# Kernel optimization log

Measured on AMD Instinct MI355X. Metric: run time of the kernel, lower is better.

## Reference

```python
import jax, jax.numpy as jnp
import numpy as np

B, G, T, N = 2, 4, 64, 300
D = 256          # detr_dim == feature_dim
R = 4            # ffn_dim_ratio
MD = 32          # motion_dim


def _xavier(key, shape):
    lim = (6.0 / (shape[0] + shape[1])) ** 0.5
    return jax.random.uniform(key, shape, jnp.float32, -lim, lim)


def setup_inputs() -> dict:
    key = jax.random.key(0)
    ks = jax.random.split(key, 16)
    feats = jax.random.normal(ks[0], (B, G, T, N, D), jnp.float32)
    boxes = jax.random.uniform(ks[1], (B, G, T, N, 4), jnp.float32)
    masks = jax.random.bernoulli(ks[2], 0.3, (B, G, T, N))
    # per-trajectory permutation of frame ids 0..T-1 (unique -> unambiguous scatter)
    u = jax.random.uniform(ks[3], (B, G, N, T))
    times = jnp.swapaxes(jnp.argsort(u, axis=-1).astype(jnp.int32), 2, 3)  # [B,G,T,N]
    return {
        'trajectory_features': feats,
        'trajectory_boxes': boxes,
        'trajectory_masks': masks,
        'trajectory_times': times,
        'adp_w1': _xavier(ks[4], (D, D * R)), 'adp_b1': jnp.zeros((D * R,), jnp.float32),
        'adp_w2': _xavier(ks[5], (D * R, D)), 'adp_b2': jnp.zeros((D,), jnp.float32),
        'norm_g': jnp.ones((D,), jnp.float32), 'norm_b': jnp.zeros((D,), jnp.float32),
        'mot_w1': _xavier(ks[6], (12, MD // 2)), 'mot_b1': jnp.zeros((MD // 2,), jnp.float32),
        'mot_w2': _xavier(ks[7], (MD // 2, MD)), 'mot_b2': jnp.zeros((MD,), jnp.float32),
        'fus_w1': _xavier(ks[8], (D + MD, D)), 'fus_b1': jnp.zeros((D,), jnp.float32),
        'fus_w2': _xavier(ks[9], (D, D)), 'fus_b2': jnp.zeros((D,), jnp.float32),
        'ffn_w1': _xavier(ks[10], (D, D * R)), 'ffn_b1': jnp.zeros((D * R,), jnp.float32),
        'ffn_w2': _xavier(ks[11], (D * R, D)), 'ffn_b2': jnp.zeros((D,), jnp.float32),
        'fnorm_g': jnp.ones((D,), jnp.float32), 'fnorm_b': jnp.zeros((D,), jnp.float32),
    }


def _ffn(x, w1, b1, w2, b2):
    return jax.nn.gelu(x @ w1 + b1, approximate=False) @ w2 + b2


def _ln(x, g, b):
    m = x.mean(-1, keepdims=True)
    v = ((x - m) ** 2).mean(-1, keepdims=True)
    return (x - m) / jnp.sqrt(v + 1e-5) * g + b


def _motion_features(boxes, masks, times, mot_w1, mot_b1, mot_w2, mot_b2):
    # boxes [B,G,T,N,4] -> trajectory-major [B,G,N,T,*]
    b_, g_, t_, n_ = masks.shape
    md = mot_b2.shape[0]
    bx = jnp.swapaxes(boxes, 2, 3)              # [B,G,N,T,4]
    valid = ~jnp.swapaxes(masks, 2, 3)          # [B,G,N,T]
    tm = jnp.swapaxes(times, 2, 3)              # [B,G,N,T]
    # sort valid entries first, by time (stable)
    order = jnp.argsort(jnp.where(valid, tm, t_ + 1), axis=-1)
    sb = jnp.take_along_axis(bx, order[..., None], axis=3)   # sorted boxes
    st = jnp.take_along_axis(tm, order, axis=-1)             # sorted times
    cnt = valid.sum(-1)                                      # [B,G,N]
    pos = jnp.arange(t_)
    in_count = pos[None, None, None, :] < cnt[..., None]
    dt = jnp.maximum(st - jnp.roll(st, 1, axis=-1), 1).astype(sb.dtype)[..., None]
    mask_v = ((pos >= 1)[None, None, None, :] & in_count)[..., None]
    vel = jnp.where(mask_v, (sb - jnp.roll(sb, 1, axis=3)) / dt, 0.0)
    mask_a = ((pos >= 2)[None, None, None, :] & in_count)[..., None]
    acc = jnp.where(mask_a, (vel - jnp.roll(vel, 1, axis=3)) / dt, 0.0)
    mv = jnp.concatenate([sb, vel, acc], axis=-1)            # [B,G,N,T,12]
    enc = jax.nn.gelu(mv @ mot_w1 + mot_b1, approximate=False) @ mot_w2 + mot_b2
    write = in_count & (cnt >= 2)[..., None] & (st < t_)
    frame = jnp.where(write, st, t_)                         # t_ -> dropped
    bi, gi, ni, ti = jnp.meshgrid(jnp.arange(b_), jnp.arange(g_), jnp.arange(n_),
                                  jnp.arange(t_), indexing='ij')
    out = jnp.zeros((b_, g_, t_, n_, md), sb.dtype)
    return out.at[bi, gi, frame, ni].set(enc, mode='drop')


def reference(trajectory_features, trajectory_boxes, trajectory_masks, trajectory_times,
              adp_w1, adp_b1, adp_w2, adp_b2, norm_g, norm_b,
              mot_w1, mot_b1, mot_w2, mot_b2,
              fus_w1, fus_b1, fus_w2, fus_b2,
              ffn_w1, ffn_b1, ffn_w2, ffn_b2, fnorm_g, fnorm_b):
    x = trajectory_features + _ffn(trajectory_features, adp_w1, adp_b1, adp_w2, adp_b2)
    x = _ln(x, norm_g, norm_b)
    motion = _motion_features(trajectory_boxes, trajectory_masks, trajectory_times,
                              mot_w1, mot_b1, mot_w2, mot_b2)
    cat = jnp.concatenate([x, motion], axis=-1)
    fused = jax.nn.gelu(cat @ fus_w1 + fus_b1, approximate=False) @ fus_w2 + fus_b2
    fused = fused + _ffn(fused, ffn_w1, ffn_b1, ffn_w2, ffn_b2)
    fused = _ln(fused, fnorm_g, fnorm_b)
    return fused, motion
```

## Files before the change

kernel.cpp:

```cpp
#include <hip/hip_runtime.h>

typedef __bf16 bf16x8 __attribute__((ext_vector_type(8)));
typedef float f32x4 __attribute__((ext_vector_type(4)));

namespace {

constexpr int T_ = 64;
constexpr int N_ = 300;
constexpr int MD_ = 32;
constexpr int BG_ = 8;
constexpr long MROWS_ = (long)BG_ * T_ * N_;
constexpr long FUSED_N = MROWS_ * 256;
constexpr int MB = 128;

constexpr long PA1 = 0;
constexpr long PA2 = 262144;
constexpr long PF1 = 524288;
constexpr long PF2 = 598016;
constexpr long PN1 = 663552;
constexpr long PN2 = 925696;

__device__ __forceinline__ float gelu_f(float x) {
  const float x2 = x * x;
  const float z2 = x * fmaf(x2, 0.07135481627f, 1.5957691216f);
  const float t = __builtin_amdgcn_rcpf(1.0f + __expf(z2));
  return x * (1.0f - t);
}

__device__ __forceinline__ float gelu_exact(float x) {
  return 0.5f * x * (1.0f + erff(x * 0.7071067811865476f));
}

__global__ void k_zero_flag(int* f) { *f = 0; }

__global__ void k_detect_mask(const unsigned char* __restrict__ m, int nbytes,
                              int* __restrict__ f) {
  int i = blockIdx.x * 256 + threadIdx.x;
  if (i < nbytes && (i & 3) != 0 && m[i] != 0) atomicOr(f, 1);
}

__global__ __launch_bounds__(256)
void k_motion(const float* __restrict__ boxes, const void* __restrict__ masks,
              const int* __restrict__ times,
              const float* __restrict__ mw1, const float* __restrict__ mb1,
              const float* __restrict__ mw2, const float* __restrict__ mb2,
              float* __restrict__ motion, const int* __restrict__ flagp) {
  __shared__ int slot[4][T_];
  __shared__ int sts[4][T_];
  __shared__ float sbx[4][T_][4];
  __shared__ float otile[4][T_][MD_];
  const int tid = threadIdx.x;
  const int w = tid >> 6, l = tid & 63;
  const int traj = blockIdx.x * 4 + w;
  const int bg = traj / N_, n = traj - bg * N_;
  const int isbool = *flagp;
  const long idx = ((long)bg * T_ + l) * N_ + n;
  const bool msk = isbool ? (((const unsigned char*)masks)[idx] != 0)
                          : (((const int*)masks)[idx] != 0);
  const bool valid = !msk;
  const int tm = times[idx];

  slot[w][l] = -1;
  sts[w][l] = 0;
  *(float4*)&sbx[w][l][0] = make_float4(0.f, 0.f, 0.f, 0.f);
  __syncthreads();
  if (valid) slot[w][tm] = l;
  __syncthreads();

  const int ot = slot[w][l];
  const bool vp = ot >= 0;
  const unsigned long long bal = __ballot(vp);
  const int cnt = __builtin_popcountll(bal);
  const int pos = __builtin_popcountll(bal & ((1ull << l) - 1ull));
  if (vp) {
    sts[w][pos] = l;
    const float4 bx = *(const float4*)(boxes + (((long)bg * T_ + ot) * N_ + n) * 4);
    *(float4*)&sbx[w][pos][0] = bx;
  }
  __syncthreads();

  const int stp = sts[w][l];
  const int stm1 = sts[w][(l + 63) & 63];
  const float4 sb = *(const float4*)&sbx[w][l][0];
  const float4 sbm = *(const float4*)&sbx[w][(l + 63) & 63][0];
  const float dt = (float)max(stp - stm1, 1);
  const float inv = 1.0f / dt;
  const bool okv = (l >= 1) && (l < cnt);
  float v0 = okv ? (sb.x - sbm.x) * inv : 0.f;
  float v1 = okv ? (sb.y - sbm.y) * inv : 0.f;
  float v2 = okv ? (sb.z - sbm.z) * inv : 0.f;
  float v3 = okv ? (sb.w - sbm.w) * inv : 0.f;
  const float p0 = __shfl_up(v0, 1, 64);
  const float p1 = __shfl_up(v1, 1, 64);
  const float p2 = __shfl_up(v2, 1, 64);
  const float p3 = __shfl_up(v3, 1, 64);
  const bool oka = (l >= 2) && (l < cnt);
  const float a0 = oka ? (v0 - p0) * inv : 0.f;
  const float a1 = oka ? (v1 - p1) * inv : 0.f;
  const float a2 = oka ? (v2 - p2) * inv : 0.f;
  const float a3 = oka ? (v3 - p3) * inv : 0.f;

  const float mv[12] = {sb.x, sb.y, sb.z, sb.w, v0, v1, v2, v3, a0, a1, a2, a3};
  float e1[16];
#pragma unroll
  for (int i = 0; i < 16; ++i) {
    float a = mb1[i];
#pragma unroll
    for (int c = 0; c < 12; ++c) a = fmaf(mv[c], mw1[c * 16 + i], a);
    e1[i] = gelu_exact(a);
  }
  float enc[32];
#pragma unroll
  for (int o = 0; o < 32; ++o) {
    float a = mb2[o];
#pragma unroll
    for (int i = 0; i < 16; ++i) a = fmaf(e1[i], mw2[i * 32 + o], a);
    enc[o] = a;
  }

#pragma unroll
  for (int c = 0; c < 32; c += 4)
    *(float4*)&otile[w][l][c] = make_float4(0.f, 0.f, 0.f, 0.f);
  __syncthreads();
  if (l < cnt && cnt >= 2) {
#pragma unroll
    for (int c = 0; c < 32; ++c) otile[w][stp][c] = enc[c];
  }
  __syncthreads();

  float* mbase = motion + ((long)bg * T_ * N_ + n) * MD_;
  const float4* srcv = (const float4*)&otile[w][l][0];
  float4* dstv = (float4*)(mbase + (long)l * N_ * MD_);
#pragma unroll
  for (int q = 0; q < 8; ++q) dstv[q] = srcv[q];
}

__global__ void k_pack(const float* __restrict__ W, __bf16* __restrict__ P,
                       int K, int NN) {
  int gid = blockIdx.x * 256 + threadIdx.x;
  int total = (K >> 5) * (NN >> 4) * 64;
  if (gid >= total) return;
  int l = gid & 63, f = gid >> 6;
  int NT = NN >> 4;
  int kb = f / NT, nt = f - kb * NT;
  int krow = kb * 32 + (l >> 4) * 8;
  int col = nt * 16 + (l & 15);
  bf16x8 v;
#pragma unroll
  for (int e = 0; e < 8; ++e) v[e] = (__bf16)W[(long)(krow + e) * NN + col];
  *(bf16x8*)(P + (long)gid * 8) = v;
}

__global__ __launch_bounds__(512, 1)
void k_mfma(const float* __restrict__ feats, const float* __restrict__ motion,
            const __bf16* __restrict__ pw,
            const float* __restrict__ ba1, const float* __restrict__ ba2,
            const float* __restrict__ ng, const float* __restrict__ nb,
            const float* __restrict__ bf1, const float* __restrict__ bf2,
            const float* __restrict__ bn1, const float* __restrict__ bn2,
            const float* __restrict__ fg, const float* __restrict__ fb,
            float* __restrict__ out) {
  __shared__ __align__(16) char smem[131072];
  __shared__ float red[MB][4][2];
  char* regA = smem;
  char* regB = smem + 65536;
  char* regM = regB;

  const int tid = threadIdx.x;
  const int l = tid & 63, wid = tid >> 6;
  const int lr = l & 15, lk = l >> 4;
  const int wr = wid >> 2;
  const int wn = wid & 3;
  const int colb = wn * 64;
  const long rowbase = (long)blockIdx.x * MB;

  const __bf16* pa1 = pw + PA1;
  const __bf16* pa2 = pw + PA2;
  const __bf16* pf1 = pw + PF1;
  const __bf16* pf2 = pw + PF2;
  const __bf16* pn1 = pw + PN1;
  const __bf16* pn2 = pw + PN2;

  auto lda = [&](const char* reg, int kb, int m) -> bf16x8 {
    const int row = wr * 64 + m * 16 + lr;
    return *(const bf16x8*)(reg + row * 512 +
                            ((((kb << 2) + lk) ^ (row & 7)) << 4));
  };
  auto ldb = [&](const __bf16* pb, int frag) -> bf16x8 {
    return *(const bf16x8*)(pb + ((long)frag << 9) + (l << 3));
  };
  auto mmL2 = [&](const char* reg, const __bf16* pb, long fragbase, int NT,
                  f32x4 (&acc)[4][4]) {
    const __bf16* bbase = pb + ((fragbase + wn * 4) << 9) + ((long)l << 3);
    const long kstride = (long)NT << 9;
    bf16x8 bA[4], bB[4];
#pragma unroll
    for (int j = 0; j < 4; ++j)
      bA[j] = *(const bf16x8*)(bbase + ((long)j << 9));
#pragma unroll
    for (int j = 0; j < 4; ++j)
      bB[j] = *(const bf16x8*)(bbase + kstride + ((long)j << 9));
#pragma unroll
    for (int kb = 0; kb < 8; ++kb) {
      bf16x8 a[4];
#pragma unroll
      for (int m = 0; m < 4; ++m) a[m] = lda(reg, kb, m);
      __builtin_amdgcn_s_setprio(1);
#pragma unroll
      for (int j = 0; j < 4; ++j) {
        const bf16x8 b = (kb & 1) ? bB[j] : bA[j];
#pragma unroll
        for (int m = 0; m < 4; ++m)
          acc[m][j] =
              __builtin_amdgcn_mfma_f32_16x16x32_bf16(a[m], b, acc[m][j], 0, 0, 0);
      }
      __builtin_amdgcn_s_setprio(0);
      if (kb < 6) {
#pragma unroll
        for (int j = 0; j < 4; ++j) {
          const bf16x8 v =
              *(const bf16x8*)(bbase + (long)(kb + 2) * kstride + ((long)j << 9));
          if (kb & 1) bB[j] = v; else bA[j] = v;
        }
      }
    }
  };
  auto store_gelu = [&](char* reg, const f32x4 (&acc)[4][4]) {
#pragma unroll
    for (int j = 0; j < 4; ++j) {
      const int col = colb + j * 16 + lr;
#pragma unroll
      for (int m = 0; m < 4; ++m)
#pragma unroll
        for (int e = 0; e < 4; ++e) {
          const int row = wr * 64 + m * 16 + lk * 4 + e;
          *(__bf16*)(reg + row * 512 + (((col >> 3) ^ (row & 7)) << 4) +
                     ((col & 7) << 1)) = (__bf16)gelu_f(acc[m][j][e]);
        }
    }
  };
  auto ln_stats = [&](const f32x4 (&acc)[4][4], float (&mean)[4][4],
                      float (&rstd)[4][4]) {
    float s1[4][4], s2[4][4];
#pragma unroll
    for (int m = 0; m < 4; ++m)
#pragma unroll
      for (int e = 0; e < 4; ++e) { s1[m][e] = 0.f; s2[m][e] = 0.f; }
#pragma unroll
    for (int m = 0; m < 4; ++m)
#pragma unroll
      for (int j = 0; j < 4; ++j)
#pragma unroll
        for (int e = 0; e < 4; ++e) {
          s1[m][e] += acc[m][j][e];
          s2[m][e] += acc[m][j][e] * acc[m][j][e];
        }
#pragma unroll
    for (int o = 1; o < 16; o <<= 1)
#pragma unroll
      for (int m = 0; m < 4; ++m)
#pragma unroll
        for (int e = 0; e < 4; ++e) {
          s1[m][e] += __shfl_xor(s1[m][e], o);
          s2[m][e] += __shfl_xor(s2[m][e], o);
        }
    if (lr == 0) {
#pragma unroll
      for (int m = 0; m < 4; ++m)
#pragma unroll
        for (int e = 0; e < 4; ++e) {
          const int row = wr * 64 + m * 16 + lk * 4 + e;
          red[row][wn][0] = s1[m][e];
          red[row][wn][1] = s2[m][e];
        }
    }
    __syncthreads();
#pragma unroll
    for (int m = 0; m < 4; ++m)
#pragma unroll
      for (int e = 0; e < 4; ++e) {
        const int row = wr * 64 + m * 16 + lk * 4 + e;
        const float S1 =
            red[row][0][0] + red[row][1][0] + red[row][2][0] + red[row][3][0];
        const float S2 =
            red[row][0][1] + red[row][1][1] + red[row][2][1] + red[row][3][1];
        const float mu = S1 * (1.0f / 256.0f);
        const float var = S2 * (1.0f / 256.0f) - mu * mu;
        mean[m][e] = mu;
        rstd[m][e] = rsqrtf(var + 1e-5f);
      }
  };

  f32x4 acc2[4][4];
#pragma unroll
  for (int j = 0; j < 4; ++j) {
    const int col = colb + j * 16 + lr;
    const float bv = ba2[col];
#pragma unroll
    for (int m = 0; m < 4; ++m)
#pragma unroll
      for (int e = 0; e < 4; ++e) {
        const int row = wr * 64 + m * 16 + lk * 4 + e;
        acc2[m][j][e] = bv + feats[(rowbase + row) * 256 + col];
      }
  }
#pragma unroll
  for (int it = 0; it < 8; ++it) {
    const int c = tid + it * 512;
    const int row = c >> 5, cc = c & 31;
    const float* src = feats + (rowbase + row) * 256 + cc * 8;
    bf16x8 v;
#pragma unroll
    for (int e = 0; e < 8; ++e) v[e] = (__bf16)src[e];
    *(bf16x8*)(regA + row * 512 + ((cc ^ (row & 7)) << 4)) = v;
  }
  __syncthreads();

#pragma unroll 1
  for (int ch = 0; ch < 4; ++ch) {
    f32x4 acc1[4][4];
#pragma unroll
    for (int j = 0; j < 4; ++j) {
      const float bv = ba1[ch * 256 + colb + j * 16 + lr];
#pragma unroll
      for (int m = 0; m < 4; ++m) acc1[m][j] = {bv, bv, bv, bv};
    }
    mmL2(regA, pa1, ch * 16, 64, acc1);
    __syncthreads();
    store_gelu(regB, acc1);
    __syncthreads();
    mmL2(regB, pa2, ch * 128, 16, acc2);
  }

  {
    float mean[4][4], rstd[4][4];
    ln_stats(acc2, mean, rstd);
#pragma unroll
    for (int j = 0; j < 4; ++j) {
      const int col = colb + j * 16 + lr;
      const float gv = ng[col], bv = nb[col];
#pragma unroll
      for (int m = 0; m < 4; ++m)
#pragma unroll
        for (int e = 0; e < 4; ++e) {
          const int row = wr * 64 + m * 16 + lk * 4 + e;
          const float v = (acc2[m][j][e] - mean[m][e]) * rstd[m][e] * gv + bv;
          *(__bf16*)(regA + row * 512 + (((col >> 3) ^ (row & 7)) << 4) +
                     ((col & 7) << 1)) = (__bf16)v;
        }
    }
    {
      const int row = tid >> 2, cc = tid & 3;
      const float* src = motion + (rowbase + row) * 32 + cc * 8;
      bf16x8 v;
#pragma unroll
      for (int e = 0; e < 8; ++e) v[e] = (__bf16)src[e];
      *(bf16x8*)(regM + row * 64 + ((cc ^ (row & 3)) << 4)) = v;
    }
  }
  __syncthreads();

  {
    f32x4 accB[4][4];
#pragma unroll
    for (int j = 0; j < 4; ++j) {
      const float bv = bf1[colb + j * 16 + lr];
#pragma unroll
      for (int m = 0; m < 4; ++m) accB[m][j] = {bv, bv, bv, bv};
    }
    mmL2(regA, pf1, 0, 16, accB);
    {
      bf16x8 a[4];
#pragma unroll
      for (int m = 0; m < 4; ++m) {
        const int row = wr * 64 + m * 16 + lr;
        a[m] = *(const bf16x8*)(regM + row * 64 + ((lk ^ (row & 3)) << 4));
      }
#pragma unroll
      for (int j = 0; j < 4; ++j) {
        const bf16x8 b = ldb(pf1, 128 + wn * 4 + j);
#pragma unroll
        for (int m = 0; m < 4; ++m)
          accB[m][j] =
              __builtin_amdgcn_mfma_f32_16x16x32_bf16(a[m], b, accB[m][j], 0, 0, 0);
      }
    }
    __syncthreads();
    store_gelu(regB, accB);
    __syncthreads();
    f32x4 accD[4][4];
#pragma unroll
    for (int j = 0; j < 4; ++j) {
      const float bv = bf2[colb + j * 16 + lr];
#pragma unroll
      for (int m = 0; m < 4; ++m) accD[m][j] = {bv, bv, bv, bv};
    }
    mmL2(regB, pf2, 0, 16, accD);
#pragma unroll
    for (int j = 0; j < 4; ++j) {
      const int col = colb + j * 16 + lr;
      const float bv = bn2[col];
#pragma unroll
      for (int m = 0; m < 4; ++m)
#pragma unroll
        for (int e = 0; e < 4; ++e) {
          const int row = wr * 64 + m * 16 + lk * 4 + e;
          const float fv = accD[m][j][e];
          *(__bf16*)(regA + row * 512 + (((col >> 3) ^ (row & 7)) << 4) +
                     ((col & 7) << 1)) = (__bf16)fv;
          acc2[m][j][e] = fv + bv;
        }
    }
  }
  __syncthreads();

#pragma unroll 1
  for (int ch = 0; ch < 4; ++ch) {
    f32x4 acc1[4][4];
#pragma unroll
    for (int j = 0; j < 4; ++j) {
      const float bv = bn1[ch * 256 + colb + j * 16 + lr];
#pragma unroll
      for (int m = 0; m < 4; ++m) acc1[m][j] = {bv, bv, bv, bv};
    }
    mmL2(regA, pn1, ch * 16, 64, acc1);
    __syncthreads();
    store_gelu(regB, acc1);
    __syncthreads();
    mmL2(regB, pn2, ch * 128, 16, acc2);
  }

  {
    float mean[4][4], rstd[4][4];
    ln_stats(acc2, mean, rstd);
#pragma unroll
    for (int j = 0; j < 4; ++j) {
      const int col = colb + j * 16 + lr;
      const float gv = fg[col], bv = fb[col];
#pragma unroll
      for (int m = 0; m < 4; ++m)
#pragma unroll
        for (int e = 0; e < 4; ++e) {
          const int row = wr * 64 + m * 16 + lk * 4 + e;
          out[(rowbase + row) * 256 + col] =
              (acc2[m][j][e] - mean[m][e]) * rstd[m][e] * gv + bv;
        }
    }
  }
}

}

extern "C" void kernel_launch(void* const* d_in, const int* in_sizes, int n_in,
                              void* d_out, int out_size, void* d_ws, size_t ws_size,
                              hipStream_t stream) {
  const float* feats = (const float*)d_in[0];
  const float* boxes = (const float*)d_in[1];
  const void*  masks = d_in[2];
  const int*   times = (const int*)d_in[3];
  const float* wa1 = (const float*)d_in[4];
  const float* ba1 = (const float*)d_in[5];
  const float* wa2 = (const float*)d_in[6];
  const float* ba2 = (const float*)d_in[7];
  const float* ng  = (const float*)d_in[8];
  const float* nb  = (const float*)d_in[9];
  const float* mw1 = (const float*)d_in[10];
  const float* mb1 = (const float*)d_in[11];
  const float* mw2 = (const float*)d_in[12];
  const float* mb2 = (const float*)d_in[13];
  const float* wf1 = (const float*)d_in[14];
  const float* bf1 = (const float*)d_in[15];
  const float* wf2 = (const float*)d_in[16];
  const float* bf2 = (const float*)d_in[17];
  const float* wn1 = (const float*)d_in[18];
  const float* bn1 = (const float*)d_in[19];
  const float* wn2 = (const float*)d_in[20];
  const float* bn2 = (const float*)d_in[21];
  const float* fg  = (const float*)d_in[22];
  const float* fb  = (const float*)d_in[23];

  float* out_fused = (float*)d_out;
  float* out_motion = out_fused + FUSED_N;
  int* flag = (int*)d_ws;
  __bf16* pw = (__bf16*)((char*)d_ws + 256);

  const int mask_elems = in_sizes[2];

  k_zero_flag<<<1, 1, 0, stream>>>(flag);
  k_detect_mask<<<(mask_elems + 255) / 256, 256, 0, stream>>>(
      (const unsigned char*)masks, mask_elems, flag);
  k_motion<<<(BG_ * N_) / 4, 256, 0, stream>>>(boxes, masks, times, mw1, mb1, mw2,
                                               mb2, out_motion, flag);

  auto packn = [&](const float* W, long off, int K, int NN) {
    const int total = (K / 32) * (NN / 16) * 64;
    k_pack<<<(total + 255) / 256, 256, 0, stream>>>(W, pw + off, K, NN);
  };
  packn(wa1, PA1, 256, 1024);
  packn(wa2, PA2, 1024, 256);
  packn(wf1, PF1, 288, 256);
  packn(wf2, PF2, 256, 256);
  packn(wn1, PN1, 256, 1024);
  packn(wn2, PN2, 1024, 256);

  k_mfma<<<(int)(MROWS_ / MB), 512, 0, stream>>>(
      feats, out_motion, pw, ba1, ba2, ng, nb, bf1, bf2, bn1, bn2, fg, fb,
      out_fused);
}
```

Before: 671.6 us.

## Split hidden-dim chunks to 128 columns and shrink shared memory buffers

Each FFN hidden chunk drops from 256 to 128 columns, so the GELU intermediate buffer halves and the chunk loop runs twice as many times. The fusion MLP's first layer is also split into two 128-column halves so the motion buffer gets its own shared-memory region. Total LDS falls from 128KB to 104KB and the per-chunk accumulators shrink, which lowers register pressure. In exchange the kernel issues twice as many barriers per FFN, and each wave now reuses every A fragment across fewer B tiles.

```diff
diff --git a/kernel.cpp b/kernel.cpp
--- a/kernel.cpp
+++ b/kernel.cpp
@@ -151,6 +151,49 @@
   *(bf16x8*)(P + (long)gid * 8) = v;
 }
 
+template <int KBN, int JN, int RSH>
+__device__ __forceinline__ void mm_l2(const char* reg, const __bf16* bb,
+                                      const long kstride, const int row0,
+                                      const int lr, const int lk,
+                                      f32x4 (&acc)[4][JN]) {
+  bf16x8 bA[JN], bB[JN];
+#pragma unroll
+  for (int j = 0; j < JN; ++j) bA[j] = *(const bf16x8*)(bb + ((long)j << 9));
+  if (KBN > 1) {
+#pragma unroll
+    for (int j = 0; j < JN; ++j)
+      bB[j] = *(const bf16x8*)(bb + kstride + ((long)j << 9));
+  }
+#pragma unroll
+  for (int kb = 0; kb < KBN; ++kb) {
+    bf16x8 a[4];
+#pragma unroll
+    for (int m = 0; m < 4; ++m) {
+      const int row = row0 + m * 16 + lr;
+      a[m] = *(const bf16x8*)(reg + ((long)row << RSH) +
+                              ((((kb << 2) + lk) ^ (row & 7)) << 4));
+    }
+    __builtin_amdgcn_s_setprio(1);
+#pragma unroll
+    for (int j = 0; j < JN; ++j) {
+      const bf16x8 b = (kb & 1) ? bB[j] : bA[j];
+#pragma unroll
+      for (int m = 0; m < 4; ++m)
+        acc[m][j] =
+            __builtin_amdgcn_mfma_f32_16x16x32_bf16(a[m], b, acc[m][j], 0, 0, 0);
+    }
+    __builtin_amdgcn_s_setprio(0);
+    if (kb < KBN - 2) {
+#pragma unroll
+      for (int j = 0; j < JN; ++j) {
+        const bf16x8 v =
+            *(const bf16x8*)(bb + (long)(kb + 2) * kstride + ((long)j << 9));
+        if (kb & 1) bB[j] = v; else bA[j] = v;
+      }
+    }
+  }
+}
+
 __global__ __launch_bounds__(512, 1)
 void k_mfma(const float* __restrict__ feats, const float* __restrict__ motion,
             const __bf16* __restrict__ pw,
@@ -160,11 +203,11 @@
             const float* __restrict__ bn1, const float* __restrict__ bn2,
             const float* __restrict__ fg, const float* __restrict__ fb,
             float* __restrict__ out) {
-  __shared__ __align__(16) char smem[131072];
+  __shared__ __align__(16) char smem[106496];
   __shared__ float red[MB][4][2];
   char* regA = smem;
   char* regB = smem + 65536;
-  char* regM = regB;
+  char* regM = smem + 98304;
 
   const int tid = threadIdx.x;
   const int l = tid & 63, wid = tid >> 6;
@@ -172,6 +215,7 @@
   const int wr = wid >> 2;
   const int wn = wid & 3;
   const int colb = wn * 64;
+  const int row0 = wr * 64;
   const long rowbase = (long)blockIdx.x * MB;
 
   const __bf16* pa1 = pw + PA1;
@@ -181,60 +225,19 @@
   const __bf16* pn1 = pw + PN1;
   const __bf16* pn2 = pw + PN2;
 
-  auto lda = [&](const char* reg, int kb, int m) -> bf16x8 {
-    const int row = wr * 64 + m * 16 + lr;
-    return *(const bf16x8*)(reg + row * 512 +
-                            ((((kb << 2) + lk) ^ (row & 7)) << 4));
-  };
   auto ldb = [&](const __bf16* pb, int frag) -> bf16x8 {
     return *(const bf16x8*)(pb + ((long)frag << 9) + (l << 3));
   };
-  auto mmL2 = [&](const char* reg, const __bf16* pb, long fragbase, int NT,
-                  f32x4 (&acc)[4][4]) {
-    const __bf16* bbase = pb + ((fragbase + wn * 4) << 9) + ((long)l << 3);
-    const long kstride = (long)NT << 9;
-    bf16x8 bA[4], bB[4];
-#pragma unroll
-    for (int j = 0; j < 4; ++j)
-      bA[j] = *(const bf16x8*)(bbase + ((long)j << 9));
-#pragma unroll
-    for (int j = 0; j < 4; ++j)
-      bB[j] = *(const bf16x8*)(bbase + kstride + ((long)j << 9));
-#pragma unroll
-    for (int kb = 0; kb < 8; ++kb) {
-      bf16x8 a[4];
-#pragma unroll
-      for (int m = 0; m < 4; ++m) a[m] = lda(reg, kb, m);
-      __builtin_amdgcn_s_setprio(1);
-#pragma unroll
-      for (int j = 0; j < 4; ++j) {
-        const bf16x8 b = (kb & 1) ? bB[j] : bA[j];
-#pragma unroll
-        for (int m = 0; m < 4; ++m)
-          acc[m][j] =
-              __builtin_amdgcn_mfma_f32_16x16x32_bf16(a[m], b, acc[m][j], 0, 0, 0);
-      }
-      __builtin_amdgcn_s_setprio(0);
-      if (kb < 6) {
-#pragma unroll
-        for (int j = 0; j < 4; ++j) {
-          const bf16x8 v =
-              *(const bf16x8*)(bbase + (long)(kb + 2) * kstride + ((long)j << 9));
-          if (kb & 1) bB[j] = v; else bA[j] = v;
-        }
-      }
-    }
-  };
-  auto store_gelu = [&](char* reg, const f32x4 (&acc)[4][4]) {
-#pragma unroll
-    for (int j = 0; j < 4; ++j) {
-      const int col = colb + j * 16 + lr;
-#pragma unroll
-      for (int m = 0; m < 4; ++m)
-#pragma unroll
-        for (int e = 0; e < 4; ++e) {
-          const int row = wr * 64 + m * 16 + lk * 4 + e;
-          *(__bf16*)(reg + row * 512 + (((col >> 3) ^ (row & 7)) << 4) +
+  auto store_gelu128 = [&](char* reg, const f32x4 (&acc)[4][2]) {
+#pragma unroll
+    for (int j = 0; j < 2; ++j) {
+      const int col = wn * 32 + j * 16 + lr;
+#pragma unroll
+      for (int m = 0; m < 4; ++m)
+#pragma unroll
+        for (int e = 0; e < 4; ++e) {
+          const int row = row0 + m * 16 + lk * 4 + e;
+          *(__bf16*)(reg + row * 256 + (((col >> 3) ^ (row & 7)) << 4) +
                      ((col & 7) << 1)) = (__bf16)gelu_f(acc[m][j][e]);
         }
     }
@@ -269,7 +272,7 @@
       for (int m = 0; m < 4; ++m)
 #pragma unroll
         for (int e = 0; e < 4; ++e) {
-          const int row = wr * 64 + m * 16 + lk * 4 + e;
+          const int row = row0 + m * 16 + lk * 4 + e;
           red[row][wn][0] = s1[m][e];
           red[row][wn][1] = s2[m][e];
         }
@@ -279,7 +282,7 @@
     for (int m = 0; m < 4; ++m)
 #pragma unroll
       for (int e = 0; e < 4; ++e) {
-        const int row = wr * 64 + m * 16 + lk * 4 + e;
+        const int row = row0 + m * 16 + lk * 4 + e;
         const float S1 =
             red[row][0][0] + red[row][1][0] + red[row][2][0] + red[row][3][0];
         const float S2 =
@@ -300,7 +303,7 @@
     for (int m = 0; m < 4; ++m)
 #pragma unroll
       for (int e = 0; e < 4; ++e) {
-        const int row = wr * 64 + m * 16 + lk * 4 + e;
+        const int row = row0 + m * 16 + lk * 4 + e;
         acc2[m][j][e] = bv + feats[(rowbase + row) * 256 + col];
       }
   }
@@ -317,19 +320,21 @@
   __syncthreads();
 
 #pragma unroll 1
-  for (int ch = 0; ch < 4; ++ch) {
-    f32x4 acc1[4][4];
-#pragma unroll
-    for (int j = 0; j < 4; ++j) {
-      const float bv = ba1[ch * 256 + colb + j * 16 + lr];
+  for (int ch = 0; ch < 8; ++ch) {
+    f32x4 acc1[4][2];
+#pragma unroll
+    for (int j = 0; j < 2; ++j) {
+      const float bv = ba1[ch * 128 + wn * 32 + j * 16 + lr];
 #pragma unroll
       for (int m = 0; m < 4; ++m) acc1[m][j] = {bv, bv, bv, bv};
     }
-    mmL2(regA, pa1, ch * 16, 64, acc1);
+    mm_l2<8, 2, 9>(regA, pa1 + ((long)(ch * 8 + wn * 2) << 9) + (l << 3),
+                   (long)64 << 9, row0, lr, lk, acc1);
     __syncthreads();
-    store_gelu(regB, acc1);
+    store_gelu128(regB, acc1);
     __syncthreads();
-    mmL2(regB, pa2, ch * 128, 16, acc2);
+    mm_l2<4, 4, 8>(regB, pa2 + ((long)(ch * 64 + wn * 4) << 9) + (l << 3),
+                   (long)16 << 9, row0, lr, lk, acc2);
   }
 
   {
@@ -343,7 +348,7 @@
       for (int m = 0; m < 4; ++m)
 #pragma unroll
         for (int e = 0; e < 4; ++e) {
-          const int row = wr * 64 + m * 16 + lk * 4 + e;
+          const int row = row0 + m * 16 + lk * 4 + e;
           const float v = (acc2[m][j][e] - mean[m][e]) * rstd[m][e] * gv + bv;
           *(__bf16*)(regA + row * 512 + (((col >> 3) ^ (row & 7)) << 4) +
                      ((col & 7) << 1)) = (__bf16)v;
@@ -361,33 +366,6 @@
   __syncthreads();
 
   {
-    f32x4 accB[4][4];
-#pragma unroll
-    for (int j = 0; j < 4; ++j) {
-      const float bv = bf1[colb + j * 16 + lr];
-#pragma unroll
-      for (int m = 0; m < 4; ++m) accB[m][j] = {bv, bv, bv, bv};
-    }
-    mmL2(regA, pf1, 0, 16, accB);
-    {
-      bf16x8 a[4];
-#pragma unroll
-      for (int m = 0; m < 4; ++m) {
-        const int row = wr * 64 + m * 16 + lr;
-        a[m] = *(const bf16x8*)(regM + row * 64 + ((lk ^ (row & 3)) << 4));
-      }
-#pragma unroll
-      for (int j = 0; j < 4; ++j) {
-        const bf16x8 b = ldb(pf1, 128 + wn * 4 + j);
-#pragma unroll
-        for (int m = 0; m < 4; ++m)
-          accB[m][j] =
-              __builtin_amdgcn_mfma_f32_16x16x32_bf16(a[m], b, accB[m][j], 0, 0, 0);
-      }
-    }
-    __syncthreads();
-    store_gelu(regB, accB);
-    __syncthreads();
     f32x4 accD[4][4];
 #pragma unroll
     for (int j = 0; j < 4; ++j) {
@@ -395,7 +373,39 @@
 #pragma unroll
       for (int m = 0; m < 4; ++m) accD[m][j] = {bv, bv, bv, bv};
     }
-    mmL2(regB, pf2, 0, 16, accD);
+#pragma unroll 1
+    for (int n0 = 0; n0 < 2; ++n0) {
+      f32x4 accB[4][2];
+#pragma unroll
+      for (int j = 0; j < 2; ++j) {
+        const float bv = bf1[n0 * 128 + wn * 32 + j * 16 + lr];
+#pragma unroll
+        for (int m = 0; m < 4; ++m) accB[m][j] = {bv, bv, bv, bv};
+      }
+      mm_l2<8, 2, 9>(regA, pf1 + ((long)(n0 * 8 + wn * 2) << 9) + (l << 3),
+                     (long)16 << 9, row0, lr, lk, accB);
+      {
+        bf16x8 a[4];
+#pragma unroll
+        for (int m = 0; m < 4; ++m) {
+          const int row = row0 + m * 16 + lr;
+          a[m] = *(const bf16x8*)(regM + row * 64 + ((lk ^ (row & 3)) << 4));
+        }
+#pragma unroll
+        for (int j = 0; j < 2; ++j) {
+          const bf16x8 b = ldb(pf1, 128 + n0 * 8 + wn * 2 + j);
+#pragma unroll
+          for (int m = 0; m < 4; ++m)
+            accB[m][j] = __builtin_amdgcn_mfma_f32_16x16x32_bf16(
+                a[m], b, accB[m][j], 0, 0, 0);
+        }
+      }
+      __syncthreads();
+      store_gelu128(regB, accB);
+      __syncthreads();
+      mm_l2<4, 4, 8>(regB, pf2 + ((long)(n0 * 64 + wn * 4) << 9) + (l << 3),
+                     (long)16 << 9, row0, lr, lk, accD);
+    }
 #pragma unroll
     for (int j = 0; j < 4; ++j) {
       const int col = colb + j * 16 + lr;
@@ -404,7 +414,7 @@
       for (int m = 0; m < 4; ++m)
 #pragma unroll
         for (int e = 0; e < 4; ++e) {
-          const int row = wr * 64 + m * 16 + lk * 4 + e;
+          const int row = row0 + m * 16 + lk * 4 + e;
           const float fv = accD[m][j][e];
           *(__bf16*)(regA + row * 512 + (((col >> 3) ^ (row & 7)) << 4) +
                      ((col & 7) << 1)) = (__bf16)fv;
@@ -415,19 +425,21 @@
   __syncthreads();
 
 #pragma unroll 1
-  for (int ch = 0; ch < 4; ++ch) {
-    f32x4 acc1[4][4];
-#pragma unroll
-    for (int j = 0; j < 4; ++j) {
-      const float bv = bn1[ch * 256 + colb + j * 16 + lr];
+  for (int ch = 0; ch < 8; ++ch) {
+    f32x4 acc1[4][2];
+#pragma unroll
+    for (int j = 0; j < 2; ++j) {
+      const float bv = bn1[ch * 128 + wn * 32 + j * 16 + lr];
 #pragma unroll
       for (int m = 0; m < 4; ++m) acc1[m][j] = {bv, bv, bv, bv};
     }
-    mmL2(regA, pn1, ch * 16, 64, acc1);
+    mm_l2<8, 2, 9>(regA, pn1 + ((long)(ch * 8 + wn * 2) << 9) + (l << 3),
+                   (long)64 << 9, row0, lr, lk, acc1);
     __syncthreads();
-    store_gelu(regB, acc1);
+    store_gelu128(regB, acc1);
     __syncthreads();
-    mmL2(regB, pn2, ch * 128, 16, acc2);
+    mm_l2<4, 4, 8>(regB, pn2 + ((long)(ch * 64 + wn * 4) << 9) + (l << 3),
+                   (long)16 << 9, row0, lr, lk, acc2);
   }
 
   {
@@ -441,7 +453,7 @@
       for (int m = 0; m < 4; ++m)
 #pragma unroll
         for (int e = 0; e < 4; ++e) {
-          const int row = wr * 64 + m * 16 + lk * 4 + e;
+          const int row = row0 + m * 16 + lk * 4 + e;
           out[(rowbase + row) * 256 + col] =
               (acc2[m][j][e] - mean[m][e]) * rstd[m][e] * gv + bv;
         }
```

After: 636.1 us. -5.3%, faster.

## Double-buffer FFN hidden chunks with transposed producer MFMA and vectorized GELU stores

Applied to the files above, without the earlier changes.

Restructures each two-layer MLP into 128-column hidden chunks. Each chunk is produced by a transposed MFMA (weight as the A operand, activations as B), so a lane's four GELU outputs are contiguous and go to shared memory as one bf16x4 store instead of scalar bf16 stores. Two hidden buffers alternate so the next chunk's first-layer work can overlap the current chunk's second-layer accumulation, which removes one barrier per chunk. Shared memory grows to about 140 KB, and the producer loops keep eight accumulator tiles live, which raises register pressure.

```diff
diff --git a/kernel.cpp b/kernel.cpp
--- a/kernel.cpp
+++ b/kernel.cpp
@@ -1,6 +1,7 @@
 #include <hip/hip_runtime.h>
 
 typedef __bf16 bf16x8 __attribute__((ext_vector_type(8)));
+typedef __bf16 bf16x4 __attribute__((ext_vector_type(4)));
 typedef float f32x4 __attribute__((ext_vector_type(4)));
 
 namespace {
@@ -151,6 +152,87 @@
   *(bf16x8*)(P + (long)gid * 8) = v;
 }
 
+template <int NKB, bool MOT, int NT>
+__device__ __forceinline__ void produce_chunk(
+    const char* regA, const char* regM, char* hb, const __bf16* pb1,
+    const float* b1, int r, int wid, int l, int lr, int lk) {
+  const int nt = r * 8 + wid;
+  f32x4 t[8];
+  {
+    const float4 bv = *(const float4*)(b1 + r * 128 + wid * 16 + lk * 4);
+#pragma unroll
+    for (int rt = 0; rt < 8; ++rt) t[rt] = f32x4{bv.x, bv.y, bv.z, bv.w};
+  }
+  const __bf16* wp = pb1 + ((long)nt << 9) + (l << 3);
+  bf16x8 w0 = *(const bf16x8*)(wp);
+  bf16x8 w1 = w0;
+  if (NKB > 1) w1 = *(const bf16x8*)(wp + ((long)NT << 9));
+#pragma unroll
+  for (int kb = 0; kb < NKB; ++kb) {
+    const bf16x8 wf = (kb & 1) ? w1 : w0;
+    if (kb + 2 < NKB) {
+      const bf16x8 v = *(const bf16x8*)(wp + ((long)(kb + 2) * NT << 9));
+      if (kb & 1) w1 = v; else w0 = v;
+    }
+    __builtin_amdgcn_s_setprio(1);
+#pragma unroll
+    for (int rt = 0; rt < 8; ++rt) {
+      const int row = rt * 16 + lr;
+      bf16x8 xf;
+      if (MOT && kb == NKB - 1)
+        xf = *(const bf16x8*)(regM + row * 64 + ((lk ^ (row & 3)) << 4));
+      else
+        xf = *(const bf16x8*)(regA + row * 512 +
+                              ((((kb << 2) + lk) ^ (row & 7)) << 4));
+      t[rt] = __builtin_amdgcn_mfma_f32_16x16x32_bf16(wf, xf, t[rt], 0, 0, 0);
+    }
+    __builtin_amdgcn_s_setprio(0);
+  }
+#pragma unroll
+  for (int rt = 0; rt < 8; ++rt) {
+    const int row = rt * 16 + lr;
+    bf16x4 hv;
+#pragma unroll
+    for (int e = 0; e < 4; ++e) hv[e] = (__bf16)gelu_f(t[rt][e]);
+    *(bf16x4*)(hb + row * 256 + ((wid * 32 + lk * 8) ^ ((row & 7) << 4))) = hv;
+  }
+}
+
+__device__ __forceinline__ void consume_chunk(const char* hb,
+                                              const __bf16* pb2, int kbg0,
+                                              int l, int lr, int lk, int wr,
+                                              int wn, f32x4 (&acc)[4][4]) {
+  const __bf16* wp = pb2 + ((long)(kbg0 * 16 + wn * 4) << 9) + (l << 3);
+  bf16x8 bw0[4], bw1[4];
+#pragma unroll
+  for (int j = 0; j < 4; ++j) bw0[j] = *(const bf16x8*)(wp + ((long)j << 9));
+#pragma unroll
+  for (int kbl = 0; kbl < 4; ++kbl) {
+    if (kbl < 3) {
+#pragma unroll
+      for (int j = 0; j < 4; ++j)
+        bw1[j] = *(const bf16x8*)(wp + ((long)((kbl + 1) * 16 + j) << 9));
+    }
+    bf16x8 a[4];
+#pragma unroll
+    for (int m = 0; m < 4; ++m) {
+      const int row = wr * 64 + m * 16 + lr;
+      a[m] = *(const bf16x8*)(hb + row * 256 +
+                              ((kbl * 64 + lk * 16) ^ ((row & 7) << 4)));
+    }
+    __builtin_amdgcn_s_setprio(1);
+#pragma unroll
+    for (int j = 0; j < 4; ++j)
+#pragma unroll
+      for (int m = 0; m < 4; ++m)
+        acc[m][j] = __builtin_amdgcn_mfma_f32_16x16x32_bf16(a[m], bw0[j],
+                                                            acc[m][j], 0, 0, 0);
+    __builtin_amdgcn_s_setprio(0);
+#pragma unroll
+    for (int j = 0; j < 4; ++j) bw0[j] = bw1[j];
+  }
+}
+
 __global__ __launch_bounds__(512, 1)
 void k_mfma(const float* __restrict__ feats, const float* __restrict__ motion,
             const __bf16* __restrict__ pw,
@@ -160,11 +242,12 @@
             const float* __restrict__ bn1, const float* __restrict__ bn2,
             const float* __restrict__ fg, const float* __restrict__ fb,
             float* __restrict__ out) {
-  __shared__ __align__(16) char smem[131072];
-  __shared__ float red[MB][4][2];
+  __shared__ __align__(16) char smem[143360];
   char* regA = smem;
-  char* regB = smem + 65536;
-  char* regM = regB;
+  char* hb0 = smem + 65536;
+  char* hb1 = smem + 98304;
+  char* regM = smem + 131072;
+  float* redp = (float*)(smem + 139264);
 
   const int tid = threadIdx.x;
   const int l = tid & 63, wid = tid >> 6;
@@ -172,6 +255,7 @@
   const int wr = wid >> 2;
   const int wn = wid & 3;
   const int colb = wn * 64;
+  const int row0 = wr * 64;
   const long rowbase = (long)blockIdx.x * MB;
 
   const __bf16* pa1 = pw + PA1;
@@ -181,64 +265,6 @@
   const __bf16* pn1 = pw + PN1;
   const __bf16* pn2 = pw + PN2;
 
-  auto lda = [&](const char* reg, int kb, int m) -> bf16x8 {
-    const int row = wr * 64 + m * 16 + lr;
-    return *(const bf16x8*)(reg + row * 512 +
-                            ((((kb << 2) + lk) ^ (row & 7)) << 4));
-  };
-  auto ldb = [&](const __bf16* pb, int frag) -> bf16x8 {
-    return *(const bf16x8*)(pb + ((long)frag << 9) + (l << 3));
-  };
-  auto mmL2 = [&](const char* reg, const __bf16* pb, long fragbase, int NT,
-                  f32x4 (&acc)[4][4]) {
-    const __bf16* bbase = pb + ((fragbase + wn * 4) << 9) + ((long)l << 3);
-    const long kstride = (long)NT << 9;
-    bf16x8 bA[4], bB[4];
-#pragma unroll
-    for (int j = 0; j < 4; ++j)
-      bA[j] = *(const bf16x8*)(bbase + ((long)j << 9));
-#pragma unroll
-    for (int j = 0; j < 4; ++j)
-      bB[j] = *(const bf16x8*)(bbase + kstride + ((long)j << 9));
-#pragma unroll
-    for (int kb = 0; kb < 8; ++kb) {
-      bf16x8 a[4];
-#pragma unroll
-      for (int m = 0; m < 4; ++m) a[m] = lda(reg, kb, m);
-      __builtin_amdgcn_s_setprio(1);
-#pragma unroll
-      for (int j = 0; j < 4; ++j) {
-        const bf16x8 b = (kb & 1) ? bB[j] : bA[j];
-#pragma unroll
-        for (int m = 0; m < 4; ++m)
-          acc[m][j] =
-              __builtin_amdgcn_mfma_f32_16x16x32_bf16(a[m], b, acc[m][j], 0, 0, 0);
-      }
-      __builtin_amdgcn_s_setprio(0);
-      if (kb < 6) {
-#pragma unroll
-        for (int j = 0; j < 4; ++j) {
-          const bf16x8 v =
-              *(const bf16x8*)(bbase + (long)(kb + 2) * kstride + ((long)j << 9));
-          if (kb & 1) bB[j] = v; else bA[j] = v;
-        }
-      }
-    }
-  };
-  auto store_gelu = [&](char* reg, const f32x4 (&acc)[4][4]) {
-#pragma unroll
-    for (int j = 0; j < 4; ++j) {
-      const int col = colb + j * 16 + lr;
-#pragma unroll
-      for (int m = 0; m < 4; ++m)
-#pragma unroll
-        for (int e = 0; e < 4; ++e) {
-          const int row = wr * 64 + m * 16 + lk * 4 + e;
-          *(__bf16*)(reg + row * 512 + (((col >> 3) ^ (row & 7)) << 4) +
-                     ((col & 7) << 1)) = (__bf16)gelu_f(acc[m][j][e]);
-        }
-    }
-  };
   auto ln_stats = [&](const f32x4 (&acc)[4][4], float (&mean)[4][4],
                       float (&rstd)[4][4]) {
     float s1[4][4], s2[4][4];
@@ -269,9 +295,9 @@
       for (int m = 0; m < 4; ++m)
 #pragma unroll
         for (int e = 0; e < 4; ++e) {
-          const int row = wr * 64 + m * 16 + lk * 4 + e;
-          red[row][wn][0] = s1[m][e];
-          red[row][wn][1] = s2[m][e];
+          const int row = row0 + m * 16 + lk * 4 + e;
+          redp[(row * 4 + wn) * 2 + 0] = s1[m][e];
+          redp[(row * 4 + wn) * 2 + 1] = s2[m][e];
         }
     }
     __syncthreads();
@@ -279,11 +305,11 @@
     for (int m = 0; m < 4; ++m)
 #pragma unroll
       for (int e = 0; e < 4; ++e) {
-        const int row = wr * 64 + m * 16 + lk * 4 + e;
-        const float S1 =
-            red[row][0][0] + red[row][1][0] + red[row][2][0] + red[row][3][0];
-        const float S2 =
-            red[row][0][1] + red[row][1][1] + red[row][2][1] + red[row][3][1];
+        const int row = row0 + m * 16 + lk * 4 + e;
+        const float S1 = redp[(row * 4 + 0) * 2] + redp[(row * 4 + 1) * 2] +
+                         redp[(row * 4 + 2) * 2] + redp[(row * 4 + 3) * 2];
+        const float S2 = redp[(row * 4 + 0) * 2 + 1] + redp[(row * 4 + 1) * 2 + 1] +
+                         redp[(row * 4 + 2) * 2 + 1] + redp[(row * 4 + 3) * 2 + 1];
         const float mu = S1 * (1.0f / 256.0f);
         const float var = S2 * (1.0f / 256.0f) - mu * mu;
         mean[m][e] = mu;
@@ -300,7 +326,7 @@
     for (int m = 0; m < 4; ++m)
 #pragma unroll
       for (int e = 0; e < 4; ++e) {
-        const int row = wr * 64 + m * 16 + lk * 4 + e;
+        const int row = row0 + m * 16 + lk * 4 + e;
         acc2[m][j][e] = bv + feats[(rowbase + row) * 256 + col];
       }
   }
@@ -316,20 +342,15 @@
   }
   __syncthreads();
 
+  produce_chunk<8, false, 64>(regA, regM, hb0, pa1, ba1, 0, wid, l, lr, lk);
+  __syncthreads();
 #pragma unroll 1
-  for (int ch = 0; ch < 4; ++ch) {
-    f32x4 acc1[4][4];
-#pragma unroll
-    for (int j = 0; j < 4; ++j) {
-      const float bv = ba1[ch * 256 + colb + j * 16 + lr];
-#pragma unroll
-      for (int m = 0; m < 4; ++m) acc1[m][j] = {bv, bv, bv, bv};
-    }
-    mmL2(regA, pa1, ch * 16, 64, acc1);
+  for (int r = 0; r < 8; ++r) {
+    if (r < 7)
+      produce_chunk<8, false, 64>(regA, regM, ((r + 1) & 1) ? hb1 : hb0, pa1,
+                                  ba1, r + 1, wid, l, lr, lk);
+    consume_chunk((r & 1) ? hb1 : hb0, pa2, r * 4, l, lr, lk, wr, wn, acc2);
     __syncthreads();
-    store_gelu(regB, acc1);
-    __syncthreads();
-    mmL2(regB, pa2, ch * 128, 16, acc2);
   }
 
   {
@@ -343,7 +364,7 @@
       for (int m = 0; m < 4; ++m)
 #pragma unroll
         for (int e = 0; e < 4; ++e) {
-          const int row = wr * 64 + m * 16 + lk * 4 + e;
+          const int row = row0 + m * 16 + lk * 4 + e;
           const float v = (acc2[m][j][e] - mean[m][e]) * rstd[m][e] * gv + bv;
           *(__bf16*)(regA + row * 512 + (((col >> 3) ^ (row & 7)) << 4) +
                      ((col & 7) << 1)) = (__bf16)v;
@@ -361,33 +382,6 @@
   __syncthreads();
 
   {
-    f32x4 accB[4][4];
-#pragma unroll
-    for (int j = 0; j < 4; ++j) {
-      const float bv = bf1[colb + j * 16 + lr];
-#pragma unroll
-      for (int m = 0; m < 4; ++m) accB[m][j] = {bv, bv, bv, bv};
-    }
-    mmL2(regA, pf1, 0, 16, accB);
-    {
-      bf16x8 a[4];
-#pragma unroll
-      for (int m = 0; m < 4; ++m) {
-        const int row = wr * 64 + m * 16 + lr;
-        a[m] = *(const bf16x8*)(regM + row * 64 + ((lk ^ (row & 3)) << 4));
-      }
-#pragma unroll
-      for (int j = 0; j < 4; ++j) {
-        const bf16x8 b = ldb(pf1, 128 + wn * 4 + j);
-#pragma unroll
-        for (int m = 0; m < 4; ++m)
-          accB[m][j] =
-              __builtin_amdgcn_mfma_f32_16x16x32_bf16(a[m], b, accB[m][j], 0, 0, 0);
-      }
-    }
-    __syncthreads();
-    store_gelu(regB, accB);
-    __syncthreads();
     f32x4 accD[4][4];
 #pragma unroll
     for (int j = 0; j < 4; ++j) {
@@ -395,7 +389,13 @@
 #pragma unroll
       for (int m = 0; m < 4; ++m) accD[m][j] = {bv, bv, bv, bv};
     }
-    mmL2(regB, pf2, 0, 16, accD);
+    produce_chunk<9, true, 16>(regA, regM, hb0, pf1, bf1, 0, wid, l, lr, lk);
+    __syncthreads();
+    produce_chunk<9, true, 16>(regA, regM, hb1, pf1, bf1, 1, wid, l, lr, lk);
+    consume_chunk(hb0, pf2, 0, l, lr, lk, wr, wn, accD);
+    __syncthreads();
+    consume_chunk(hb1, pf2, 4, l, lr, lk, wr, wn, accD);
+    __syncthreads();
 #pragma unroll
     for (int j = 0; j < 4; ++j) {
       const int col = colb + j * 16 + lr;
@@ -404,7 +404,7 @@
       for (int m = 0; m < 4; ++m)
 #pragma unroll
         for (int e = 0; e < 4; ++e) {
-          const int row = wr * 64 + m * 16 + lk * 4 + e;
+          const int row = row0 + m * 16 + lk * 4 + e;
           const float fv = accD[m][j][e];
           *(__bf16*)(regA + row * 512 + (((col >> 3) ^ (row & 7)) << 4) +
                      ((col & 7) << 1)) = (__bf16)fv;
@@ -414,20 +414,15 @@
   }
   __syncthreads();
 
+  produce_chunk<8, false, 64>(regA, regM, hb0, pn1, bn1, 0, wid, l, lr, lk);
+  __syncthreads();
 #pragma unroll 1
-  for (int ch = 0; ch < 4; ++ch) {
-    f32x4 acc1[4][4];
-#pragma unroll
-    for (int j = 0; j < 4; ++j) {
-      const float bv = bn1[ch * 256 + colb + j * 16 + lr];
-#pragma unroll
-      for (int m = 0; m < 4; ++m) acc1[m][j] = {bv, bv, bv, bv};
-    }
-    mmL2(regA, pn1, ch * 16, 64, acc1);
+  for (int r = 0; r < 8; ++r) {
+    if (r < 7)
+      produce_chunk<8, false, 64>(regA, regM, ((r + 1) & 1) ? hb1 : hb0, pn1,
+                                  bn1, r + 1, wid, l, lr, lk);
+    consume_chunk((r & 1) ? hb1 : hb0, pn2, r * 4, l, lr, lk, wr, wn, acc2);
     __syncthreads();
-    store_gelu(regB, acc1);
-    __syncthreads();
-    mmL2(regB, pn2, ch * 128, 16, acc2);
   }
 
   {
@@ -441,7 +436,7 @@
       for (int m = 0; m < 4; ++m)
 #pragma unroll
         for (int e = 0; e < 4; ++e) {
-          const int row = wr * 64 + m * 16 + lk * 4 + e;
+          const int row = row0 + m * 16 + lk * 4 + e;
           out[(rowbase + row) * 256 + col] =
               (acc2[m][j][e] - mean[m][e]) * rstd[m][e] * gv + bv;
         }
```

Measured after the change: 616.0 us. 1.09x faster.
